# Optimization experiments

Hardware: AMD Instinct MI355X
Metric: run time of the kernel (lower is better)

The kernel has to match this reference:

```python
import jax, jax.numpy as jnp
import numpy as np

E, H, I, B, K = 8, 2048, 5632, 1024, 2


def setup_inputs() -> dict:
    key = jax.random.key(0)
    k_x, k_id, k_w, k_g, k_u, k_d = jax.random.split(key, 6)
    x = jax.random.normal(k_x, (B, H), dtype=jnp.float32)
    expert_ids = jax.random.randint(k_id, (B, K), 0, E).astype(jnp.int32)
    ew = jax.random.uniform(k_w, (B, K), dtype=jnp.float32)
    expert_weights = ew / jnp.sum(ew, axis=-1, keepdims=True)  # router probs, sum to 1
    scale = 0.02
    gate_weights = jax.random.normal(k_g, (E, H, I), dtype=jnp.float32) * scale
    up_weights = jax.random.normal(k_u, (E, H, I), dtype=jnp.float32) * scale
    down_weights = jax.random.normal(k_d, (E, I, H), dtype=jnp.float32) * scale
    return {
        "x": x,
        "expert_ids": expert_ids,
        "expert_weights": expert_weights,
        "gate_weights": gate_weights,
        "up_weights": up_weights,
        "down_weights": down_weights,
    }


def reference(x, expert_ids, expert_weights, gate_weights, up_weights, down_weights):
    # Faithful math: per token t, expert e = expert_ids[t,k]:
    #   out[t] = sum_k expert_weights[t,k] * (silu(x W_gate_e) * (x W_up_e)) W_down_e
    # Implemented as dense all-expert GEMMs + select, which computes the
    # identical per-expert matmuls as the original's gathered-weight einsums
    # without materializing the [B,K,H,I] gathered weight tensor.
    gate_all = jnp.einsum('bh,ehi->bei', x, gate_weights)        # [B,E,I]
    up_all = jnp.einsum('bh,ehi->bei', x, up_weights)            # [B,E,I]
    act_all = jax.nn.silu(gate_all) * up_all                     # [B,E,I]
    out_all = jnp.einsum('bei,eih->beh', act_all, down_weights)  # [B,E,H]
    # Select the top_k experts' outputs per token: [B,K,H]
    sel = jnp.take_along_axis(out_all, expert_ids[:, :, None], axis=1)
    return jnp.sum(sel * expert_weights[:, :, None], axis=1)     # [B,H]
```

## Files before the change

### kernel.cpp

```cpp
#include <hip/hip_runtime.h>
#include <hip/hip_bf16.h>

#define E_ 8
#define H_ 2048
#define I_ 5632
#define B_ 1024
#define K_ 2
#define NROWS (B_*K_)

#define BM 128
#define BN 64
#define BK 64
#define MAXT 24
#define NKG (H_/BK)
#define NKD (I_/BK)
#define NYG (I_/BN)
#define NYD (H_/BN)

typedef __attribute__((ext_vector_type(8))) __bf16 bf16x8;
typedef __attribute__((ext_vector_type(4))) float f32x4;

union BF4 { __bf16 b[4]; uint2 q; };
union BF8 { __bf16 b[8]; uint4 q; };

__device__ __forceinline__ void gld_lds16(const void* g, void* l) {
  __builtin_amdgcn_global_load_lds(
      (const __attribute__((address_space(1))) void*)g,
      (__attribute__((address_space(3))) void*)l, 16, 0, 0);
}

#define GLOAD4(dst, ptr) asm volatile("global_load_dwordx4 %0, %1, off" : "=v"(dst) : "v"(ptr))
#define WAITV(N) do { asm volatile("s_waitcnt vmcnt(" #N ")" ::: "memory"); __builtin_amdgcn_sched_barrier(0); } while(0)
#define WAITL()  do { asm volatile("s_waitcnt lgkmcnt(0)" ::: "memory"); __builtin_amdgcn_sched_barrier(0); } while(0)
#define BAR()    __builtin_amdgcn_s_barrier()

#define MSK(c) (((c)&7) ^ (((c)>>2)&7))

__global__ void cvtx_kernel(const float* __restrict__ x, __bf16* __restrict__ xb) {
  int i = (blockIdx.x * 256 + threadIdx.x) * 8;
  float4 a = *(const float4*)(x + i);
  float4 b = *(const float4*)(x + i + 4);
  BF8 r;
  r.b[0] = (__bf16)a.x; r.b[1] = (__bf16)a.y; r.b[2] = (__bf16)a.z; r.b[3] = (__bf16)a.w;
  r.b[4] = (__bf16)b.x; r.b[5] = (__bf16)b.y; r.b[6] = (__bf16)b.z; r.b[7] = (__bf16)b.w;
  *(uint4*)(xb + i) = r.q;
}

__global__ void route_kernel(const int* __restrict__ ids,
                             int* __restrict__ counts, int* __restrict__ offsets,
                             int* __restrict__ tlist, int* __restrict__ row_of,
                             int* __restrict__ tile_e, int* __restrict__ tile_m) {
  __shared__ int sc[E_], sp[E_], so[E_];
  int t = threadIdx.x;
  if (t < E_) { sc[t] = 0; sp[t] = 0; }
  __syncthreads();
  for (int idx = t; idx < NROWS; idx += 256) atomicAdd(&sc[ids[idx]], 1);
  __syncthreads();
  if (t == 0) {
    int acc = 0;
    for (int e = 0; e < E_; ++e) { so[e] = acc; acc += sc[e]; }
    int nt = 0;
    for (int e = 0; e < E_; ++e)
      for (int m0 = 0; m0 < sc[e]; m0 += BM) { tile_e[nt] = e; tile_m[nt] = m0; ++nt; }
    for (; nt < MAXT; ++nt) { tile_e[nt] = 0; tile_m[nt] = 0x7FFFFFFF; }
  }
  __syncthreads();
  for (int idx = t; idx < NROWS; idx += 256) {
    int e = ids[idx];
    int slot = atomicAdd(&sp[e], 1);
    int row = so[e] + slot;
    tlist[row] = idx / K_;
    row_of[idx] = row;
  }
  if (t < E_) { counts[t] = sc[t]; offsets[t] = so[t]; }
}

__global__ __launch_bounds__(256, 2) void gateup_kernel(
    const __bf16* __restrict__ xb, const float* __restrict__ gw,
    const float* __restrict__ uw, const int* __restrict__ counts,
    const int* __restrict__ offsets, const int* __restrict__ tlist,
    const int* __restrict__ tile_e, const int* __restrict__ tile_m,
    __bf16* __restrict__ act)
{
  extern __shared__ char smem[];
  char* As0 = smem;
  char* As1 = smem + 16384;
  char* Bg0 = smem + 32768;
  char* Bg1 = smem + 40960;
  char* Bu0 = smem + 49152;
  char* Bu1 = smem + 57344;

  const int id = blockIdx.x;
  const int w  = (id & 7) * 264 + (id >> 3);
  const int tt = w % MAXT;
  const int ny = w / MAXT;
  const int e  = tile_e[tt];
  const int m0 = tile_m[tt];
  const int cnt = counts[e];
  if (m0 >= cnt) return;
  const int off = offsets[e];
  const int n0 = ny * BN;

  const int tid  = threadIdx.x;
  const int lane = tid & 63;
  const int wave = tid >> 6;
  const int wr = (wave >> 1) * 64;
  const int wc = (wave & 1) * 32;

  const __bf16* asrc0; const __bf16* asrc1; const __bf16* asrc2; const __bf16* asrc3;
  int ad0, ad1, ad2, ad3;
  {
    const __bf16* s[4]; int d[4];
#pragma unroll
    for (int i = 0; i < 4; ++i) {
      int f = i*256 + tid;
      int r = f >> 3, cs = f & 7;
      int rr = m0 + r; if (rr >= cnt) rr = cnt - 1;
      int tok = tlist[off + rr];
      s[i] = xb + (size_t)tok * H_ + ((cs ^ (r & 7)) << 3);
      d[i] = f * 16;
    }
    asrc0=s[0]; asrc1=s[1]; asrc2=s[2]; asrc3=s[3];
    ad0=d[0]; ad1=d[1]; ad2=d[2]; ad3=d[3];
  }

  const int cq = tid & 15;
  const int kb = (tid >> 4) * 4;
  const float* pg0 = gw + ((size_t)e*H_ + kb + 0)*I_ + n0 + 4*cq;
  const float* pg1 = gw + ((size_t)e*H_ + kb + 1)*I_ + n0 + 4*cq;
  const float* pg2 = gw + ((size_t)e*H_ + kb + 2)*I_ + n0 + 4*cq;
  const float* pg3 = gw + ((size_t)e*H_ + kb + 3)*I_ + n0 + 4*cq;
  const float* pu0 = uw + ((size_t)e*H_ + kb + 0)*I_ + n0 + 4*cq;
  const float* pu1 = uw + ((size_t)e*H_ + kb + 1)*I_ + n0 + 4*cq;
  const float* pu2 = uw + ((size_t)e*H_ + kb + 2)*I_ + n0 + 4*cq;
  const float* pu3 = uw + ((size_t)e*H_ + kb + 3)*I_ + n0 + 4*cq;
  const int slot = kb >> 3;
  const int half = (kb & 4) << 1;
  int bw0, bw1, bw2, bw3;
  {
    int b[4];
#pragma unroll
    for (int i = 0; i < 4; ++i) {
      int c = 4*cq + i;
      b[i] = c*128 + ((slot ^ MSK(c)) << 4) + half;
    }
    bw0=b[0]; bw1=b[1]; bw2=b[2]; bw3=b[3];
  }

  f32x4 vgA_0,vgA_1,vgA_2,vgA_3, vuA_0,vuA_1,vuA_2,vuA_3;
  f32x4 vgB_0,vgB_1,vgB_2,vgB_3, vuB_0,vuB_1,vuB_2,vuB_3;

  f32x4 accg[4][2], accu[4][2];
#pragma unroll
  for (int i = 0; i < 4; ++i)
#pragma unroll
    for (int j = 0; j < 2; ++j) {
      accg[i][j] = (f32x4){0.f,0.f,0.f,0.f};
      accu[i][j] = (f32x4){0.f,0.f,0.f,0.f};
    }

  auto COMPUTE = [&](const char* Ab, const char* Bgb, const char* Bub) {
#pragma unroll
    for (int kk = 0; kk < 2; ++kk) {
      const int ks = kk*4 + (lane >> 4);
      const int r0 = wr + (lane & 15);
      const int swa = (ks ^ (r0 & 7)) << 4;
      bf16x8 a0 = *(const bf16x8*)(Ab + (r0 +  0)*128 + swa);
      bf16x8 a1 = *(const bf16x8*)(Ab + (r0 + 16)*128 + swa);
      bf16x8 a2 = *(const bf16x8*)(Ab + (r0 + 32)*128 + swa);
      bf16x8 a3 = *(const bf16x8*)(Ab + (r0 + 48)*128 + swa);
      const int c0 = wc + (lane & 15);
      const int swb0 = (ks ^ MSK(c0)) << 4;
      const int swb1 = swb0 ^ (4 << 4);
      bf16x8 g0 = *(const bf16x8*)(Bgb + c0*128 + swb0);
      bf16x8 g1 = *(const bf16x8*)(Bgb + (c0+16)*128 + swb1);
      bf16x8 u0 = *(const bf16x8*)(Bub + c0*128 + swb0);
      bf16x8 u1 = *(const bf16x8*)(Bub + (c0+16)*128 + swb1);
      accg[0][0] = __builtin_amdgcn_mfma_f32_16x16x32_bf16(a0, g0, accg[0][0], 0,0,0);
      accg[1][0] = __builtin_amdgcn_mfma_f32_16x16x32_bf16(a1, g0, accg[1][0], 0,0,0);
      accg[2][0] = __builtin_amdgcn_mfma_f32_16x16x32_bf16(a2, g0, accg[2][0], 0,0,0);
      accg[3][0] = __builtin_amdgcn_mfma_f32_16x16x32_bf16(a3, g0, accg[3][0], 0,0,0);
      accg[0][1] = __builtin_amdgcn_mfma_f32_16x16x32_bf16(a0, g1, accg[0][1], 0,0,0);
      accg[1][1] = __builtin_amdgcn_mfma_f32_16x16x32_bf16(a1, g1, accg[1][1], 0,0,0);
      accg[2][1] = __builtin_amdgcn_mfma_f32_16x16x32_bf16(a2, g1, accg[2][1], 0,0,0);
      accg[3][1] = __builtin_amdgcn_mfma_f32_16x16x32_bf16(a3, g1, accg[3][1], 0,0,0);
      accu[0][0] = __builtin_amdgcn_mfma_f32_16x16x32_bf16(a0, u0, accu[0][0], 0,0,0);
      accu[1][0] = __builtin_amdgcn_mfma_f32_16x16x32_bf16(a1, u0, accu[1][0], 0,0,0);
      accu[2][0] = __builtin_amdgcn_mfma_f32_16x16x32_bf16(a2, u0, accu[2][0], 0,0,0);
      accu[3][0] = __builtin_amdgcn_mfma_f32_16x16x32_bf16(a3, u0, accu[3][0], 0,0,0);
      accu[0][1] = __builtin_amdgcn_mfma_f32_16x16x32_bf16(a0, u1, accu[0][1], 0,0,0);
      accu[1][1] = __builtin_amdgcn_mfma_f32_16x16x32_bf16(a1, u1, accu[1][1], 0,0,0);
      accu[2][1] = __builtin_amdgcn_mfma_f32_16x16x32_bf16(a2, u1, accu[2][1], 0,0,0);
      accu[3][1] = __builtin_amdgcn_mfma_f32_16x16x32_bf16(a3, u1, accu[3][1], 0,0,0);
    }
  };

#define GU_PF(S, KPF) do { size_t o_ = (size_t)(KPF)*(size_t)BK*(size_t)I_; \
    GLOAD4(vg##S##_0, pg0+o_); GLOAD4(vu##S##_0, pu0+o_); \
    GLOAD4(vg##S##_1, pg1+o_); GLOAD4(vu##S##_1, pu1+o_); \
    GLOAD4(vg##S##_2, pg2+o_); GLOAD4(vu##S##_2, pu2+o_); \
    GLOAD4(vg##S##_3, pg3+o_); GLOAD4(vu##S##_3, pu3+o_); } while(0)

#define GU_CVW1(BG, V0, V1, V2, V3, BWI, I) do { BF4 p_; \
    p_.b[0]=(__bf16)V0[I]; p_.b[1]=(__bf16)V1[I]; p_.b[2]=(__bf16)V2[I]; p_.b[3]=(__bf16)V3[I]; \
    *(uint2*)((BG)+BWI) = p_.q; } while(0)

#define GU_CVW(S, BG, BU) do { \
    GU_CVW1(BG, vg##S##_0, vg##S##_1, vg##S##_2, vg##S##_3, bw0, 0); \
    GU_CVW1(BG, vg##S##_0, vg##S##_1, vg##S##_2, vg##S##_3, bw1, 1); \
    GU_CVW1(BG, vg##S##_0, vg##S##_1, vg##S##_2, vg##S##_3, bw2, 2); \
    GU_CVW1(BG, vg##S##_0, vg##S##_1, vg##S##_2, vg##S##_3, bw3, 3); \
    GU_CVW1(BU, vu##S##_0, vu##S##_1, vu##S##_2, vu##S##_3, bw0, 0); \
    GU_CVW1(BU, vu##S##_0, vu##S##_1, vu##S##_2, vu##S##_3, bw1, 1); \
    GU_CVW1(BU, vu##S##_0, vu##S##_1, vu##S##_2, vu##S##_3, bw2, 2); \
    GU_CVW1(BU, vu##S##_0, vu##S##_1, vu##S##_2, vu##S##_3, bw3, 3); } while(0)

#define GU_GLDA(DST, KPF) do { size_t k_ = (size_t)(KPF)*(size_t)BK; \
    gld_lds16(asrc0 + k_, (DST)+ad0); gld_lds16(asrc1 + k_, (DST)+ad1); \
    gld_lds16(asrc2 + k_, (DST)+ad2); gld_lds16(asrc3 + k_, (DST)+ad3); } while(0)

  GU_PF(A, 0);
  GU_GLDA(As0, 0);
  WAITV(4);
  GU_CVW(A, Bg0, Bu0);
  GU_PF(B, 1);
  GU_GLDA(As1, 1);
  WAITV(12);
  WAITL();
  BAR();

#pragma unroll 1
  for (int kt = 0; kt < NKG; kt += 2) {
    {
      int kpf = kt + 2; if (kpf > NKG-1) kpf = NKG-1;
      GU_PF(A, kpf);
      COMPUTE(As0, Bg0, Bu0);
      WAITV(12);
      GU_CVW(B, Bg1, Bu1);
      WAITV(8);
      WAITL();
      BAR();
      GU_GLDA(As0, kpf);
    }
    {
      int kpf = kt + 3; if (kpf > NKG-1) kpf = NKG-1;
      GU_PF(B, kpf);
      COMPUTE(As1, Bg1, Bu1);
      WAITV(12);
      GU_CVW(A, Bg0, Bu0);
      WAITV(8);
      WAITL();
      BAR();
      GU_GLDA(As1, kpf);
    }
  }
  WAITV(0);
  WAITL();

  const int rsub = (lane >> 4) * 4;
  const int csub = lane & 15;
#pragma unroll
  for (int mi = 0; mi < 4; ++mi)
#pragma unroll
    for (int j = 0; j < 4; ++j) {
      int rl = wr + mi*16 + rsub + j;
      if (m0 + rl < cnt) {
        size_t orow = (size_t)(off + m0 + rl) * I_ + n0 + wc + csub;
#pragma unroll
        for (int cg = 0; cg < 2; ++cg) {
          float g = accg[mi][cg][j];
          float u = accu[mi][cg][j];
          float sg = g / (1.0f + __expf(-g));
          act[orow + cg*16] = (__bf16)(sg * u);
        }
      }
    }
#undef GU_PF
#undef GU_CVW
#undef GU_CVW1
#undef GU_GLDA
}

__global__ __launch_bounds__(256, 3) void down_kernel(
    const __bf16* __restrict__ act, const float* __restrict__ dw,
    const int* __restrict__ counts, const int* __restrict__ offsets,
    const int* __restrict__ tile_e, const int* __restrict__ tile_m,
    float* __restrict__ rowbuf)
{
  extern __shared__ char smem[];
  char* As0 = smem;
  char* As1 = smem + 16384;
  char* Bs0 = smem + 32768;
  char* Bs1 = smem + 40960;

  const int id = blockIdx.x;
  const int w  = (id & 7) * 96 + (id >> 3);
  const int tt = w % MAXT;
  const int ny = w / MAXT;
  const int e  = tile_e[tt];
  const int m0 = tile_m[tt];
  const int cnt = counts[e];
  if (m0 >= cnt) return;
  const int off = offsets[e];
  const int n0 = ny * BN;

  const int tid  = threadIdx.x;
  const int lane = tid & 63;
  const int wave = tid >> 6;
  const int wr = (wave >> 1) * 64;
  const int wc = (wave & 1) * 32;

  const __bf16* asrc0; const __bf16* asrc1; const __bf16* asrc2; const __bf16* asrc3;
  int ad0, ad1, ad2, ad3;
  {
    const __bf16* s[4]; int d[4];
#pragma unroll
    for (int i = 0; i < 4; ++i) {
      int f = i*256 + tid;
      int r = f >> 3, cs = f & 7;
      int rr = m0 + r; if (rr >= cnt) rr = cnt - 1;
      s[i] = act + (size_t)(off + rr) * I_ + ((cs ^ (r & 7)) << 3);
      d[i] = f * 16;
    }
    asrc0=s[0]; asrc1=s[1]; asrc2=s[2]; asrc3=s[3];
    ad0=d[0]; ad1=d[1]; ad2=d[2]; ad3=d[3];
  }

  const int cq = tid & 15;
  const int kb = (tid >> 4) * 4;
  const float* pd0 = dw + ((size_t)e*I_ + kb + 0)*H_ + n0 + 4*cq;
  const float* pd1 = dw + ((size_t)e*I_ + kb + 1)*H_ + n0 + 4*cq;
  const float* pd2 = dw + ((size_t)e*I_ + kb + 2)*H_ + n0 + 4*cq;
  const float* pd3 = dw + ((size_t)e*I_ + kb + 3)*H_ + n0 + 4*cq;
  const int slot = kb >> 3;
  const int half = (kb & 4) << 1;
  int bw0, bw1, bw2, bw3;
  {
    int b[4];
#pragma unroll
    for (int i = 0; i < 4; ++i) {
      int c = 4*cq + i;
      b[i] = c*128 + ((slot ^ MSK(c)) << 4) + half;
    }
    bw0=b[0]; bw1=b[1]; bw2=b[2]; bw3=b[3];
  }

  f32x4 vdA_0,vdA_1,vdA_2,vdA_3;
  f32x4 vdB_0,vdB_1,vdB_2,vdB_3;

  f32x4 acc[4][2];
#pragma unroll
  for (int i = 0; i < 4; ++i)
#pragma unroll
    for (int j = 0; j < 2; ++j) acc[i][j] = (f32x4){0.f,0.f,0.f,0.f};

  auto COMPUTE = [&](const char* Ab, const char* Bb) {
#pragma unroll
    for (int kk = 0; kk < 2; ++kk) {
      const int ks = kk*4 + (lane >> 4);
      const int r0 = wr + (lane & 15);
      const int swa = (ks ^ (r0 & 7)) << 4;
      bf16x8 a0 = *(const bf16x8*)(Ab + (r0 +  0)*128 + swa);
      bf16x8 a1 = *(const bf16x8*)(Ab + (r0 + 16)*128 + swa);
      bf16x8 a2 = *(const bf16x8*)(Ab + (r0 + 32)*128 + swa);
      bf16x8 a3 = *(const bf16x8*)(Ab + (r0 + 48)*128 + swa);
      const int c0 = wc + (lane & 15);
      const int swb0 = (ks ^ MSK(c0)) << 4;
      const int swb1 = swb0 ^ (4 << 4);
      bf16x8 b0 = *(const bf16x8*)(Bb + c0*128 + swb0);
      bf16x8 b1 = *(const bf16x8*)(Bb + (c0+16)*128 + swb1);
      acc[0][0] = __builtin_amdgcn_mfma_f32_16x16x32_bf16(a0, b0, acc[0][0], 0,0,0);
      acc[1][0] = __builtin_amdgcn_mfma_f32_16x16x32_bf16(a1, b0, acc[1][0], 0,0,0);
      acc[2][0] = __builtin_amdgcn_mfma_f32_16x16x32_bf16(a2, b0, acc[2][0], 0,0,0);
      acc[3][0] = __builtin_amdgcn_mfma_f32_16x16x32_bf16(a3, b0, acc[3][0], 0,0,0);
      acc[0][1] = __builtin_amdgcn_mfma_f32_16x16x32_bf16(a0, b1, acc[0][1], 0,0,0);
      acc[1][1] = __builtin_amdgcn_mfma_f32_16x16x32_bf16(a1, b1, acc[1][1], 0,0,0);
      acc[2][1] = __builtin_amdgcn_mfma_f32_16x16x32_bf16(a2, b1, acc[2][1], 0,0,0);
      acc[3][1] = __builtin_amdgcn_mfma_f32_16x16x32_bf16(a3, b1, acc[3][1], 0,0,0);
    }
  };

#define DN_PF(S, KPF) do { size_t o_ = (size_t)(KPF)*(size_t)BK*(size_t)H_; \
    GLOAD4(vd##S##_0, pd0+o_); GLOAD4(vd##S##_1, pd1+o_); \
    GLOAD4(vd##S##_2, pd2+o_); GLOAD4(vd##S##_3, pd3+o_); } while(0)

#define DN_CVW1(BB, V0, V1, V2, V3, BWI, I) do { BF4 p_; \
    p_.b[0]=(__bf16)V0[I]; p_.b[1]=(__bf16)V1[I]; p_.b[2]=(__bf16)V2[I]; p_.b[3]=(__bf16)V3[I]; \
    *(uint2*)((BB)+BWI) = p_.q; } while(0)

#define DN_CVW(S, BB) do { \
    DN_CVW1(BB, vd##S##_0, vd##S##_1, vd##S##_2, vd##S##_3, bw0, 0); \
    DN_CVW1(BB, vd##S##_0, vd##S##_1, vd##S##_2, vd##S##_3, bw1, 1); \
    DN_CVW1(BB, vd##S##_0, vd##S##_1, vd##S##_2, vd##S##_3, bw2, 2); \
    DN_CVW1(BB, vd##S##_0, vd##S##_1, vd##S##_2, vd##S##_3, bw3, 3); } while(0)

#define DN_GLDA(DST, KPF) do { size_t k_ = (size_t)(KPF)*(size_t)BK; \
    gld_lds16(asrc0 + k_, (DST)+ad0); gld_lds16(asrc1 + k_, (DST)+ad1); \
    gld_lds16(asrc2 + k_, (DST)+ad2); gld_lds16(asrc3 + k_, (DST)+ad3); } while(0)

  DN_PF(A, 0);
  DN_GLDA(As0, 0);
  WAITV(4);
  DN_CVW(A, Bs0);
  DN_PF(B, 1);
  DN_GLDA(As1, 1);
  WAITV(8);
  WAITL();
  BAR();

#pragma unroll 1
  for (int kt = 0; kt < NKD; kt += 2) {
    {
      int kpf = kt + 2; if (kpf > NKD-1) kpf = NKD-1;
      DN_PF(A, kpf);
      COMPUTE(As0, Bs0);
      WAITV(8);
      DN_CVW(B, Bs1);
      WAITV(4);
      WAITL();
      BAR();
      DN_GLDA(As0, kpf);
    }
    {
      int kpf = kt + 3; if (kpf > NKD-1) kpf = NKD-1;
      DN_PF(B, kpf);
      COMPUTE(As1, Bs1);
      WAITV(8);
      DN_CVW(A, Bs0);
      WAITV(4);
      WAITL();
      BAR();
      DN_GLDA(As1, kpf);
    }
  }
  WAITV(0);
  WAITL();

  const int rsub = (lane >> 4) * 4;
  const int csub = lane & 15;
#pragma unroll
  for (int mi = 0; mi < 4; ++mi)
#pragma unroll
    for (int j = 0; j < 4; ++j) {
      int rl = wr + mi*16 + rsub + j;
      if (m0 + rl < cnt) {
        size_t orow = (size_t)(off + m0 + rl) * H_ + n0 + wc + csub;
#pragma unroll
        for (int cg = 0; cg < 2; ++cg)
          rowbuf[orow + cg*16] = acc[mi][cg][j];
      }
    }
#undef DN_PF
#undef DN_CVW
#undef DN_CVW1
#undef DN_GLDA
}

__global__ void combine_kernel(const float* __restrict__ ew, const int* __restrict__ row_of,
                               const float* __restrict__ rowbuf, float* __restrict__ out) {
  int idx = blockIdx.x * 256 + threadIdx.x;
  int t  = idx >> 9;
  int h4 = idx & 511;
  float w0 = ew[t*2+0], w1 = ew[t*2+1];
  int r0 = row_of[t*2+0], r1 = row_of[t*2+1];
  float4 a = *(const float4*)(rowbuf + (size_t)r0*H_ + h4*4);
  float4 b = *(const float4*)(rowbuf + (size_t)r1*H_ + h4*4);
  float4 o;
  o.x = w0*a.x + w1*b.x; o.y = w0*a.y + w1*b.y;
  o.z = w0*a.z + w1*b.z; o.w = w0*a.w + w1*b.w;
  *(float4*)(out + (size_t)idx*4) = o;
}

extern "C" void kernel_launch(void* const* d_in, const int* in_sizes, int n_in,
                              void* d_out, int out_size, void* d_ws, size_t ws_size,
                              hipStream_t stream) {
  const float* x   = (const float*)d_in[0];
  const int*   ids = (const int*)d_in[1];
  const float* ew  = (const float*)d_in[2];
  const float* gw  = (const float*)d_in[3];
  const float* uw  = (const float*)d_in[4];
  const float* dwn = (const float*)d_in[5];
  float* out = (float*)d_out;

  char* ws = (char*)d_ws;
  int* counts  = (int*)ws;
  int* offsets = counts + 8;
  int* tlist   = offsets + 8;
  int* row_of  = tlist + NROWS;
  int* tile_e  = row_of + NROWS;
  int* tile_m  = tile_e + MAXT;
  __bf16* xb   = (__bf16*)(ws + 32768);
  __bf16* act  = (__bf16*)(ws + 32768 + (size_t)B_*H_*2);
  float* rowbuf = (float*)(ws + 32768 + (size_t)B_*H_*2 + (size_t)NROWS*I_*2);

  hipFuncSetAttribute(reinterpret_cast<const void*>(&gateup_kernel),
                      hipFuncAttributeMaxDynamicSharedMemorySize, 65536);
  hipFuncSetAttribute(reinterpret_cast<const void*>(&down_kernel),
                      hipFuncAttributeMaxDynamicSharedMemorySize, 49152);

  cvtx_kernel<<<B_*H_/(256*8), 256, 0, stream>>>(x, xb);
  route_kernel<<<1, 256, 0, stream>>>(ids, counts, offsets, tlist, row_of, tile_e, tile_m);

  gateup_kernel<<<MAXT*NYG, 256, 65536, stream>>>(xb, gw, uw, counts, offsets, tlist,
                                                  tile_e, tile_m, act);

  down_kernel<<<MAXT*NYD, 256, 49152, stream>>>(act, dwn, counts, offsets,
                                                tile_e, tile_m, rowbuf);

  combine_kernel<<<(B_*H_/4)/256, 256, 0, stream>>>(ew, row_of, rowbuf, out);
}
```

Before: 415.1 us.

## Single-buffer gate/up weight tiles in LDS to raise occupancy, prioritize MFMA waves

The gate/up kernel drops from double-buffered to single-buffered B tiles for the gate and up weights. This cuts shared memory from 64KB to 48KB and halves the prefetch register sets, so launch bounds can rise to 3 blocks per CU. The main loop now computes, waits, barriers, converts and stores the next weight tile, then issues the following prefetch, which adds an extra barrier per step and less overlap within a block. s_setprio is raised around the MFMA sections in both GEMM kernels to favour waves that are issuing matrix ops.

```diff
diff --git a/kernel.cpp b/kernel.cpp
--- a/kernel.cpp
+++ b/kernel.cpp
@@ -75,7 +75,7 @@
   if (t < E_) { counts[t] = sc[t]; offsets[t] = so[t]; }
 }
 
-__global__ __launch_bounds__(256, 2) void gateup_kernel(
+__global__ __launch_bounds__(256, 3) void gateup_kernel(
     const __bf16* __restrict__ xb, const float* __restrict__ gw,
     const float* __restrict__ uw, const int* __restrict__ counts,
     const int* __restrict__ offsets, const int* __restrict__ tlist,
@@ -85,10 +85,8 @@
   extern __shared__ char smem[];
   char* As0 = smem;
   char* As1 = smem + 16384;
-  char* Bg0 = smem + 32768;
-  char* Bg1 = smem + 40960;
-  char* Bu0 = smem + 49152;
-  char* Bu1 = smem + 57344;
+  char* Bg  = smem + 32768;
+  char* Bu  = smem + 40960;
 
   const int id = blockIdx.x;
   const int w  = (id & 7) * 264 + (id >> 3);
@@ -147,8 +145,7 @@
     bw0=b[0]; bw1=b[1]; bw2=b[2]; bw3=b[3];
   }
 
-  f32x4 vgA_0,vgA_1,vgA_2,vgA_3, vuA_0,vuA_1,vuA_2,vuA_3;
-  f32x4 vgB_0,vgB_1,vgB_2,vgB_3, vuB_0,vuB_1,vuB_2,vuB_3;
+  f32x4 vg_0,vg_1,vg_2,vg_3, vu_0,vu_1,vu_2,vu_3;
 
   f32x4 accg[4][2], accu[4][2];
 #pragma unroll
@@ -159,7 +156,8 @@
       accu[i][j] = (f32x4){0.f,0.f,0.f,0.f};
     }
 
-  auto COMPUTE = [&](const char* Ab, const char* Bgb, const char* Bub) {
+  auto COMPUTE = [&](const char* Ab) {
+    __builtin_amdgcn_s_setprio(1);
 #pragma unroll
     for (int kk = 0; kk < 2; ++kk) {
       const int ks = kk*4 + (lane >> 4);
@@ -172,10 +170,10 @@
       const int c0 = wc + (lane & 15);
       const int swb0 = (ks ^ MSK(c0)) << 4;
       const int swb1 = swb0 ^ (4 << 4);
-      bf16x8 g0 = *(const bf16x8*)(Bgb + c0*128 + swb0);
-      bf16x8 g1 = *(const bf16x8*)(Bgb + (c0+16)*128 + swb1);
-      bf16x8 u0 = *(const bf16x8*)(Bub + c0*128 + swb0);
-      bf16x8 u1 = *(const bf16x8*)(Bub + (c0+16)*128 + swb1);
+      bf16x8 g0 = *(const bf16x8*)(Bg + c0*128 + swb0);
+      bf16x8 g1 = *(const bf16x8*)(Bg + (c0+16)*128 + swb1);
+      bf16x8 u0 = *(const bf16x8*)(Bu + c0*128 + swb0);
+      bf16x8 u1 = *(const bf16x8*)(Bu + (c0+16)*128 + swb1);
       accg[0][0] = __builtin_amdgcn_mfma_f32_16x16x32_bf16(a0, g0, accg[0][0], 0,0,0);
       accg[1][0] = __builtin_amdgcn_mfma_f32_16x16x32_bf16(a1, g0, accg[1][0], 0,0,0);
       accg[2][0] = __builtin_amdgcn_mfma_f32_16x16x32_bf16(a2, g0, accg[2][0], 0,0,0);
@@ -193,39 +191,40 @@
       accu[2][1] = __builtin_amdgcn_mfma_f32_16x16x32_bf16(a2, u1, accu[2][1], 0,0,0);
       accu[3][1] = __builtin_amdgcn_mfma_f32_16x16x32_bf16(a3, u1, accu[3][1], 0,0,0);
     }
+    __builtin_amdgcn_s_setprio(0);
   };
 
-#define GU_PF(S, KPF) do { size_t o_ = (size_t)(KPF)*(size_t)BK*(size_t)I_; \
-    GLOAD4(vg##S##_0, pg0+o_); GLOAD4(vu##S##_0, pu0+o_); \
-    GLOAD4(vg##S##_1, pg1+o_); GLOAD4(vu##S##_1, pu1+o_); \
-    GLOAD4(vg##S##_2, pg2+o_); GLOAD4(vu##S##_2, pu2+o_); \
-    GLOAD4(vg##S##_3, pg3+o_); GLOAD4(vu##S##_3, pu3+o_); } while(0)
-
-#define GU_CVW1(BG, V0, V1, V2, V3, BWI, I) do { BF4 p_; \
+#define GU_PF(KPF) do { size_t o_ = (size_t)(KPF)*(size_t)BK*(size_t)I_; \
+    GLOAD4(vg_0, pg0+o_); GLOAD4(vu_0, pu0+o_); \
+    GLOAD4(vg_1, pg1+o_); GLOAD4(vu_1, pu1+o_); \
+    GLOAD4(vg_2, pg2+o_); GLOAD4(vu_2, pu2+o_); \
+    GLOAD4(vg_3, pg3+o_); GLOAD4(vu_3, pu3+o_); } while(0)
+
+#define GU_CVW1(BB, V0, V1, V2, V3, BWI, I) do { BF4 p_; \
     p_.b[0]=(__bf16)V0[I]; p_.b[1]=(__bf16)V1[I]; p_.b[2]=(__bf16)V2[I]; p_.b[3]=(__bf16)V3[I]; \
-    *(uint2*)((BG)+BWI) = p_.q; } while(0)
-
-#define GU_CVW(S, BG, BU) do { \
-    GU_CVW1(BG, vg##S##_0, vg##S##_1, vg##S##_2, vg##S##_3, bw0, 0); \
-    GU_CVW1(BG, vg##S##_0, vg##S##_1, vg##S##_2, vg##S##_3, bw1, 1); \
-    GU_CVW1(BG, vg##S##_0, vg##S##_1, vg##S##_2, vg##S##_3, bw2, 2); \
-    GU_CVW1(BG, vg##S##_0, vg##S##_1, vg##S##_2, vg##S##_3, bw3, 3); \
-    GU_CVW1(BU, vu##S##_0, vu##S##_1, vu##S##_2, vu##S##_3, bw0, 0); \
-    GU_CVW1(BU, vu##S##_0, vu##S##_1, vu##S##_2, vu##S##_3, bw1, 1); \
-    GU_CVW1(BU, vu##S##_0, vu##S##_1, vu##S##_2, vu##S##_3, bw2, 2); \
-    GU_CVW1(BU, vu##S##_0, vu##S##_1, vu##S##_2, vu##S##_3, bw3, 3); } while(0)
+    *(uint2*)((BB)+BWI) = p_.q; } while(0)
+
+#define GU_CVW() do { \
+    GU_CVW1(Bg, vg_0, vg_1, vg_2, vg_3, bw0, 0); \
+    GU_CVW1(Bg, vg_0, vg_1, vg_2, vg_3, bw1, 1); \
+    GU_CVW1(Bg, vg_0, vg_1, vg_2, vg_3, bw2, 2); \
+    GU_CVW1(Bg, vg_0, vg_1, vg_2, vg_3, bw3, 3); \
+    GU_CVW1(Bu, vu_0, vu_1, vu_2, vu_3, bw0, 0); \
+    GU_CVW1(Bu, vu_0, vu_1, vu_2, vu_3, bw1, 1); \
+    GU_CVW1(Bu, vu_0, vu_1, vu_2, vu_3, bw2, 2); \
+    GU_CVW1(Bu, vu_0, vu_1, vu_2, vu_3, bw3, 3); } while(0)
 
 #define GU_GLDA(DST, KPF) do { size_t k_ = (size_t)(KPF)*(size_t)BK; \
     gld_lds16(asrc0 + k_, (DST)+ad0); gld_lds16(asrc1 + k_, (DST)+ad1); \
     gld_lds16(asrc2 + k_, (DST)+ad2); gld_lds16(asrc3 + k_, (DST)+ad3); } while(0)
 
-  GU_PF(A, 0);
+  GU_PF(0);
+  WAITV(0);
+  GU_CVW();
   GU_GLDA(As0, 0);
-  WAITV(4);
-  GU_CVW(A, Bg0, Bu0);
-  GU_PF(B, 1);
+  WAITV(0);
+  GU_PF(1);
   GU_GLDA(As1, 1);
-  WAITV(12);
   WAITL();
   BAR();
 
@@ -233,10 +232,12 @@
   for (int kt = 0; kt < NKG; kt += 2) {
     {
       int kpf = kt + 2; if (kpf > NKG-1) kpf = NKG-1;
-      GU_PF(A, kpf);
-      COMPUTE(As0, Bg0, Bu0);
-      WAITV(12);
-      GU_CVW(B, Bg1, Bu1);
+      COMPUTE(As0);
+      WAITV(4);
+      WAITL();
+      BAR();
+      GU_CVW();
+      GU_PF(kpf);
       WAITV(8);
       WAITL();
       BAR();
@@ -244,10 +245,12 @@
     }
     {
       int kpf = kt + 3; if (kpf > NKG-1) kpf = NKG-1;
-      GU_PF(B, kpf);
-      COMPUTE(As1, Bg1, Bu1);
-      WAITV(12);
-      GU_CVW(A, Bg0, Bu0);
+      COMPUTE(As1);
+      WAITV(4);
+      WAITL();
+      BAR();
+      GU_CVW();
+      GU_PF(kpf);
       WAITV(8);
       WAITL();
       BAR();
@@ -355,6 +358,7 @@
     for (int j = 0; j < 2; ++j) acc[i][j] = (f32x4){0.f,0.f,0.f,0.f};
 
   auto COMPUTE = [&](const char* Ab, const char* Bb) {
+    __builtin_amdgcn_s_setprio(1);
 #pragma unroll
     for (int kk = 0; kk < 2; ++kk) {
       const int ks = kk*4 + (lane >> 4);
@@ -378,6 +382,7 @@
       acc[2][1] = __builtin_amdgcn_mfma_f32_16x16x32_bf16(a2, b1, acc[2][1], 0,0,0);
       acc[3][1] = __builtin_amdgcn_mfma_f32_16x16x32_bf16(a3, b1, acc[3][1], 0,0,0);
     }
+    __builtin_amdgcn_s_setprio(0);
   };
 
 #define DN_PF(S, KPF) do { size_t o_ = (size_t)(KPF)*(size_t)BK*(size_t)H_; \
@@ -494,14 +499,14 @@
   float* rowbuf = (float*)(ws + 32768 + (size_t)B_*H_*2 + (size_t)NROWS*I_*2);
 
   hipFuncSetAttribute(reinterpret_cast<const void*>(&gateup_kernel),
-                      hipFuncAttributeMaxDynamicSharedMemorySize, 65536);
+                      hipFuncAttributeMaxDynamicSharedMemorySize, 49152);
   hipFuncSetAttribute(reinterpret_cast<const void*>(&down_kernel),
                       hipFuncAttributeMaxDynamicSharedMemorySize, 49152);
 
   cvtx_kernel<<<B_*H_/(256*8), 256, 0, stream>>>(x, xb);
   route_kernel<<<1, 256, 0, stream>>>(ids, counts, offsets, tlist, row_of, tile_e, tile_m);
 
-  gateup_kernel<<<MAXT*NYG, 256, 65536, stream>>>(xb, gw, uw, counts, offsets, tlist,
+  gateup_kernel<<<MAXT*NYG, 256, 49152, stream>>>(xb, gw, uw, counts, offsets, tlist,
                                                   tile_e, tile_m, act);
 
   down_kernel<<<MAXT*NYD, 256, 49152, stream>>>(act, dwn, counts, offsets,
```

Result: no change. 419.9 us (+1.2%).
